# Performance work log

Hardware: AMD Instinct MI355X
Metric: run time of the kernel (lower is better)

The kernel has to match this reference:

```python
import jax, jax.numpy as jnp
import numpy as np

N = 50000
E = 800000
IN, EMB1, EMB2, L1 = 256, 128, 64, 64
EPS = 1e-8


def leaky_relu(x, slope=0.2):
    return jnp.where(x > 0, x, slope * x)


def graph_conv(x, row, col, w_rel, w_root, b):
    # torch_geometric GraphConv with sum aggregation:
    # out = (A @ x) @ w_rel^T + b + x @ w_root^T, where (A @ x)[r] = sum_{e: row[e]=r} x[col[e]]
    agg = jax.ops.segment_sum(x[col], row, num_segments=N)
    return agg @ w_rel.T + x @ w_root.T + b


def setup_inputs() -> dict:
    key = jax.random.key(0)
    ks = jax.random.split(key, 24)
    def g(k, shape, scale=0.05):
        return jax.random.normal(k, shape, dtype=jnp.float32) * scale
    return {
        "x": jax.random.normal(ks[0], (N, IN), dtype=jnp.float32),
        "row": jax.random.randint(ks[1], (E,), 0, N),
        "col": jax.random.randint(ks[2], (E,), 0, N),
        "w_rel1": g(ks[3], (EMB1, IN)), "w_root1": g(ks[4], (EMB1, IN)), "b1": g(ks[5], (EMB1,)),
        "w_rel_mu": g(ks[6], (EMB2, EMB1)), "w_root_mu": g(ks[7], (EMB2, EMB1)), "b_mu": g(ks[8], (EMB2,)),
        "w_std": g(ks[9], (EMB2, EMB1)), "b_std": g(ks[10], (EMB2,)),
        "w_rel_g1": g(ks[11], (L1, EMB2)), "w_root_g1": g(ks[12], (L1, EMB2)), "b_g1": g(ks[13], (L1,)),
        "w_rel_g2": g(ks[14], (1, L1)), "w_root_g2": g(ks[15], (1, L1)), "b_g2": g(ks[16], (1,)),
        "w_cls1": g(ks[17], (L1, EMB2)), "b_cls1": g(ks[18], (L1,)),
        "w_cls2": g(ks[19], (2, L1)), "b_cls2": g(ks[20], (2,)),
        "log_std": jnp.zeros((1,), dtype=jnp.float32),
    }


def reference(x, row, col,
              w_rel1, w_root1, b1,
              w_rel_mu, w_root_mu, b_mu,
              w_std, b_std,
              w_rel_g1, w_root_g1, b_g1,
              w_rel_g2, w_root_g2, b_g2,
              w_cls1, b_cls1, w_cls2, b_cls2, log_std):
    # ----- encode -----
    h = leaky_relu(graph_conv(x, row, col, w_rel1, w_root1, b1))  # [N, EMB1]
    z_mu = jnp.tanh(graph_conv(h, row, col, w_rel_mu, w_root_mu, b_mu))  # [N, EMB2]
    z_log_std = jnp.tanh(h @ w_std.T + b_std)                    # [N, EMB2]
    z_std = jnp.exp(z_log_std)
    z = z_mu  # eval mode
    # ----- decode: per-edge cosine similarity -----
    a, b = z[row], z[col]                                        # [E, EMB2]
    num = jnp.sum(a * b, axis=-1)
    na = jnp.maximum(jnp.linalg.norm(a, axis=-1), EPS)
    nb = jnp.maximum(jnp.linalg.norm(b, axis=-1), EPS)
    w_mu = num / (na * nb)                                       # [E]
    w_std_out = jnp.exp(log_std)                                 # [1]
    # ----- attention pooling -----
    g1 = leaky_relu(graph_conv(z, row, col, w_rel_g1, w_root_g1, b_g1))  # [N, L1]
    gate = graph_conv(g1, row, col, w_rel_g2, w_root_g2, b_g2)   # [N, 1]
    gate = jax.nn.softmax(gate, axis=0)
    pooled = gate.T @ z                                          # [1, EMB2]
    # ----- classifier -----
    y = leaky_relu(pooled @ w_cls1.T + b_cls1)
    y = y @ w_cls2.T + b_cls2
    y = jax.nn.softmax(y, axis=1)                                # [1, 2]
    return (y, w_mu, w_std_out, z, z_mu, z_std)
```

## Files before the change

kernel.cpp:

```cpp
#include <hip/hip_runtime.h>

#define NN 50000
#define EE 800000

__global__ void hist_k(const int* __restrict__ row, int* __restrict__ deg, int E) {
    int e = blockIdx.x * blockDim.x + threadIdx.x;
    if (e < E) atomicAdd(&deg[row[e]], 1);
}

__global__ __launch_bounds__(1024) void scan_k(const int* __restrict__ deg, int* __restrict__ ptr,
                                               int* __restrict__ cursor, int N) {
    __shared__ int sm[1024];
    int t = threadIdx.x;
    int chunk = (N + 1023) / 1024;
    int lo = t * chunk, hi = lo + chunk; if (hi > N) hi = N;
    int s = 0;
    for (int i = lo; i < hi; i++) s += deg[i];
    sm[t] = s;
    __syncthreads();
    for (int off = 1; off < 1024; off <<= 1) {
        int v = (t >= off) ? sm[t - off] : 0;
        __syncthreads();
        sm[t] += v;
        __syncthreads();
    }
    int run = (t == 0) ? 0 : sm[t - 1];
    for (int i = lo; i < hi; i++) { ptr[i] = run; cursor[i] = run; run += deg[i]; }
    if (t == 1023) ptr[N] = sm[1023];
}

__global__ void place_k(const int* __restrict__ row, const int* __restrict__ col,
                        int* __restrict__ cursor, int* __restrict__ ccol, int E) {
    int e = blockIdx.x * blockDim.x + threadIdx.x;
    if (e >= E) return;
    int p = atomicAdd(&cursor[row[e]], 1);
    ccol[p] = col[e];
}

__global__ void transpose_all(const float* __restrict__ w_rel1, const float* __restrict__ w_root1,
                              const float* __restrict__ w_rel_mu, const float* __restrict__ w_root_mu,
                              const float* __restrict__ w_std,
                              const float* __restrict__ w_rel_g1, const float* __restrict__ w_root_g1,
                              float* __restrict__ wt1, float* __restrict__ wt3,
                              float* __restrict__ wtg) {
    int idx = blockIdx.x * 256 + threadIdx.x;
    if (idx < 65536) {
        int j = idx & 255, k = idx >> 8;
        wt1[idx] = (j < 128) ? w_rel1[j * 256 + k] : w_root1[(j - 128) * 256 + k];
    } else if (idx < 90112) {
        int o = idx - 65536; int j = o % 192, k = o / 192;
        wt3[o] = (j < 64) ? w_rel_mu[j * 128 + k]
               : (j < 128) ? w_root_mu[(j - 64) * 128 + k]
                           : w_std[(j - 128) * 128 + k];
    } else if (idx < 98304) {
        int o = idx - 90112; int j = o & 127, k = o >> 7;
        wtg[o] = (j < 64) ? w_rel_g1[j * 64 + k] : w_root_g1[(j - 64) * 64 + k];
    }
}

__global__ __launch_bounds__(64) void mm256_k(const float* __restrict__ x,
        const float* __restrict__ wt,
        float* __restrict__ xr, float* __restrict__ xroot) {
    int t = threadIdx.x;
    int n0 = blockIdx.x * 8;
    const float* xp = x + (size_t)n0 * 256;
    float a0[8] = {}, a1[8] = {}, a2[8] = {}, a3[8] = {};
#pragma unroll 4
    for (int k = 0; k < 256; k++) {
        const float* wk = wt + k * 256;
        float w0 = wk[t], w1 = wk[t + 64], w2 = wk[t + 128], w3 = wk[t + 192];
#pragma unroll
        for (int n = 0; n < 8; n++) {
            float xv = xp[n * 256 + k];
            a0[n] = fmaf(xv, w0, a0[n]);
            a1[n] = fmaf(xv, w1, a1[n]);
            a2[n] = fmaf(xv, w2, a2[n]);
            a3[n] = fmaf(xv, w3, a3[n]);
        }
    }
#pragma unroll
    for (int n = 0; n < 8; n++) {
        size_t o = (size_t)(n0 + n) * 128;
        xr[o + t]        = a0[n];
        xr[o + t + 64]   = a1[n];
        xroot[o + t]      = a2[n];
        xroot[o + t + 64] = a3[n];
    }
}

__global__ __launch_bounds__(128) void agg_k128(const float* __restrict__ src,
        const int* __restrict__ ptr, const int* __restrict__ ccol, float* __restrict__ dst) {
    int r = blockIdx.x, j = threadIdx.x;
    int beg = ptr[r], end = ptr[r + 1];
    float a0 = 0.f, a1 = 0.f, a2 = 0.f, a3 = 0.f;
    int e = beg;
    for (; e + 4 <= end; e += 4) {
        int c0 = ccol[e], c1 = ccol[e + 1], c2 = ccol[e + 2], c3 = ccol[e + 3];
        a0 += src[(size_t)c0 * 128 + j];
        a1 += src[(size_t)c1 * 128 + j];
        a2 += src[(size_t)c2 * 128 + j];
        a3 += src[(size_t)c3 * 128 + j];
    }
    for (; e < end; e++) a0 += src[(size_t)ccol[e] * 128 + j];
    dst[(size_t)r * 128 + j] = (a0 + a1) + (a2 + a3);
}

__global__ __launch_bounds__(256) void h_k(const float4* __restrict__ agg1,
        const float4* __restrict__ xroot, const float* __restrict__ b1,
        float4* __restrict__ h, int total4) {
    int i = blockIdx.x * 256 + threadIdx.x;
    if (i >= total4) return;
    float4 a = agg1[i], x = xroot[i];
    int k = (i & 31) * 4;
    float4 r;
    r.x = a.x + x.x + b1[k + 0]; r.x = r.x > 0.f ? r.x : 0.2f * r.x;
    r.y = a.y + x.y + b1[k + 1]; r.y = r.y > 0.f ? r.y : 0.2f * r.y;
    r.z = a.z + x.z + b1[k + 2]; r.z = r.z > 0.f ? r.z : 0.2f * r.z;
    r.w = a.w + x.w + b1[k + 3]; r.w = r.w > 0.f ? r.w : 0.2f * r.w;
    h[i] = r;
}

__global__ __launch_bounds__(64) void mm128x3_k(const float* __restrict__ h,
        const float* __restrict__ wt,
        float* __restrict__ hr, float* __restrict__ hmu, float* __restrict__ hstd) {
    int t = threadIdx.x;
    int n0 = blockIdx.x * 8;
    const float* hp = h + (size_t)n0 * 128;
    float a0[8] = {}, a1[8] = {}, a2[8] = {};
#pragma unroll 4
    for (int k = 0; k < 128; k++) {
        const float* wk = wt + k * 192;
        float w0 = wk[t], w1 = wk[t + 64], w2 = wk[t + 128];
#pragma unroll
        for (int n = 0; n < 8; n++) {
            float hv = hp[n * 128 + k];
            a0[n] = fmaf(hv, w0, a0[n]);
            a1[n] = fmaf(hv, w1, a1[n]);
            a2[n] = fmaf(hv, w2, a2[n]);
        }
    }
#pragma unroll
    for (int n = 0; n < 8; n++) {
        size_t o = (size_t)(n0 + n) * 64 + t;
        hr[o] = a0[n]; hmu[o] = a1[n]; hstd[o] = a2[n];
    }
}

__global__ __launch_bounds__(64) void aggz_k(const float* __restrict__ hr,
        const float* __restrict__ hmu, const float* __restrict__ hstd,
        const float* __restrict__ b_mu, const float* __restrict__ b_std,
        const int* __restrict__ ptr, const int* __restrict__ ccol,
        float* __restrict__ z, float* __restrict__ out_z, float* __restrict__ out_zmu,
        float* __restrict__ out_zstd, float* __restrict__ nrm) {
    int r = blockIdx.x, j = threadIdx.x;
    int beg = ptr[r], end = ptr[r + 1];
    float a0 = 0.f, a1 = 0.f, a2 = 0.f, a3 = 0.f;
    int e = beg;
    for (; e + 4 <= end; e += 4) {
        int c0 = ccol[e], c1 = ccol[e + 1], c2 = ccol[e + 2], c3 = ccol[e + 3];
        a0 += hr[(size_t)c0 * 64 + j];
        a1 += hr[(size_t)c1 * 64 + j];
        a2 += hr[(size_t)c2 * 64 + j];
        a3 += hr[(size_t)c3 * 64 + j];
    }
    for (; e < end; e++) a0 += hr[(size_t)ccol[e] * 64 + j];
    float acc = (a0 + a1) + (a2 + a3);
    float zmu = tanhf(acc + hmu[(size_t)r * 64 + j] + b_mu[j]);
    float zls = tanhf(hstd[(size_t)r * 64 + j] + b_std[j]);
    float zstd = expf(zls);
    size_t o = (size_t)r * 64 + j;
    z[o] = zmu; out_z[o] = zmu; out_zmu[o] = zmu; out_zstd[o] = zstd;
    float s = zmu * zmu;
    s += __shfl_xor(s, 1); s += __shfl_xor(s, 2); s += __shfl_xor(s, 4);
    s += __shfl_xor(s, 8); s += __shfl_xor(s, 16); s += __shfl_xor(s, 32);
    if (j == 0) nrm[r] = fmaxf(sqrtf(s), 1e-8f);
}

__global__ __launch_bounds__(256) void edge_k(const float* __restrict__ z, const float* __restrict__ nrm,
        const int* __restrict__ row, const int* __restrict__ col, float* __restrict__ out, int E) {
    int t = threadIdx.x;
    int sub = t >> 4, off = t & 15;
    int e = blockIdx.x * 16 + sub;
    if (e >= E) return;
    int r = row[e], c = col[e];
    const float4* a = reinterpret_cast<const float4*>(z + (size_t)r * 64);
    const float4* b = reinterpret_cast<const float4*>(z + (size_t)c * 64);
    float4 av = a[off], bv = b[off];
    float s = av.x * bv.x + av.y * bv.y + av.z * bv.z + av.w * bv.w;
    s += __shfl_xor(s, 1); s += __shfl_xor(s, 2); s += __shfl_xor(s, 4); s += __shfl_xor(s, 8);
    if (off == 0) out[e] = s / (nrm[r] * nrm[c]);
}

__global__ __launch_bounds__(64) void mm64x2_k(const float* __restrict__ z,
        const float* __restrict__ wt,
        float* __restrict__ zr, float* __restrict__ zroot) {
    int t = threadIdx.x;
    int n0 = blockIdx.x * 8;
    const float* zp = z + (size_t)n0 * 64;
    float a0[8] = {}, a1[8] = {};
#pragma unroll 4
    for (int k = 0; k < 64; k++) {
        const float* wk = wt + k * 128;
        float w0 = wk[t], w1 = wk[t + 64];
#pragma unroll
        for (int n = 0; n < 8; n++) {
            float zv = zp[n * 64 + k];
            a0[n] = fmaf(zv, w0, a0[n]);
            a1[n] = fmaf(zv, w1, a1[n]);
        }
    }
#pragma unroll
    for (int n = 0; n < 8; n++) {
        size_t o = (size_t)(n0 + n) * 64 + t;
        zr[o] = a0[n]; zroot[o] = a1[n];
    }
}

__global__ __launch_bounds__(64) void g1gate_k(const float* __restrict__ zr, const float* __restrict__ zroot,
        const float* __restrict__ b_g1, const float* __restrict__ w_rel_g2,
        const float* __restrict__ w_root_g2,
        const int* __restrict__ ptr, const int* __restrict__ ccol,
        float* __restrict__ g1r, float* __restrict__ groot) {
    int r = blockIdx.x, j = threadIdx.x;
    int beg = ptr[r], end = ptr[r + 1];
    float a0 = 0.f, a1 = 0.f, a2 = 0.f, a3 = 0.f;
    int e = beg;
    for (; e + 4 <= end; e += 4) {
        int c0 = ccol[e], c1 = ccol[e + 1], c2 = ccol[e + 2], c3 = ccol[e + 3];
        a0 += zr[(size_t)c0 * 64 + j];
        a1 += zr[(size_t)c1 * 64 + j];
        a2 += zr[(size_t)c2 * 64 + j];
        a3 += zr[(size_t)c3 * 64 + j];
    }
    for (; e < end; e++) a0 += zr[(size_t)ccol[e] * 64 + j];
    float g = (a0 + a1) + (a2 + a3) + zroot[(size_t)r * 64 + j] + b_g1[j];
    g = g > 0.f ? g : 0.2f * g;
    float sr = g * w_rel_g2[j];
    float so = g * w_root_g2[j];
    sr += __shfl_xor(sr, 1); sr += __shfl_xor(sr, 2); sr += __shfl_xor(sr, 4);
    sr += __shfl_xor(sr, 8); sr += __shfl_xor(sr, 16); sr += __shfl_xor(sr, 32);
    so += __shfl_xor(so, 1); so += __shfl_xor(so, 2); so += __shfl_xor(so, 4);
    so += __shfl_xor(so, 8); so += __shfl_xor(so, 16); so += __shfl_xor(so, 32);
    if (j == 0) { g1r[r] = sr; groot[r] = so; }
}

__global__ __launch_bounds__(256) void gateagg_k(const float* __restrict__ g1r,
        const float* __restrict__ groot, const float* __restrict__ b_g2,
        const int* __restrict__ ptr, const int* __restrict__ ccol,
        float* __restrict__ gate, float* __restrict__ pmax, int N) {
    __shared__ float sm[256];
    float b = b_g2[0];
    float m = -3.4e38f;
    for (int r = blockIdx.x * blockDim.x + threadIdx.x; r < N; r += gridDim.x * blockDim.x) {
        int beg = ptr[r], end = ptr[r + 1];
        float s0 = 0.f, s1 = 0.f, s2 = 0.f, s3 = 0.f;
        int e = beg;
        for (; e + 4 <= end; e += 4) {
            s0 += g1r[ccol[e]]; s1 += g1r[ccol[e + 1]];
            s2 += g1r[ccol[e + 2]]; s3 += g1r[ccol[e + 3]];
        }
        for (; e < end; e++) s0 += g1r[ccol[e]];
        float g = (s0 + s1) + (s2 + s3) + groot[r] + b;
        gate[r] = g;
        m = fmaxf(m, g);
    }
    sm[threadIdx.x] = m;
    __syncthreads();
    for (int s2 = 128; s2 > 0; s2 >>= 1) {
        if (threadIdx.x < s2) sm[threadIdx.x] = fmaxf(sm[threadIdx.x], sm[threadIdx.x + s2]);
        __syncthreads();
    }
    if (threadIdx.x == 0) pmax[blockIdx.x] = sm[0];
}

__global__ void reduce_max_final(const float* __restrict__ pmax, float* __restrict__ smax) {
    float m = pmax[threadIdx.x];
    for (int o = 32; o > 0; o >>= 1) m = fmaxf(m, __shfl_down(m, o));
    if (threadIdx.x == 0) smax[0] = m;
}

__global__ __launch_bounds__(256) void pooled_kernel(const float* __restrict__ gate,
        const float* __restrict__ smax, const float* __restrict__ z,
        float* __restrict__ pooled_num, float* __restrict__ wsum, int N) {
    int tid = threadIdx.x;
    int sub = tid >> 6, j = tid & 63;
    float mx = smax[0];
    float acc = 0.f, wsl = 0.f;
    for (int n = blockIdx.x * 4 + sub; n < N; n += gridDim.x * 4) {
        float w = expf(gate[n] - mx);
        acc = fmaf(w, z[(size_t)n * 64 + j], acc);
        if (j == 0) wsl += w;
    }
    __shared__ float lp[4][64];
    __shared__ float lw[4];
    lp[sub][j] = acc;
    if (j == 0) lw[sub] = wsl;
    __syncthreads();
    if (sub == 0) {
        float t = lp[0][j] + lp[1][j] + lp[2][j] + lp[3][j];
        atomicAdd(&pooled_num[j], t);
        if (j == 0) atomicAdd(wsum, lw[0] + lw[1] + lw[2] + lw[3]);
    }
}

__global__ void final_kernel(const float* __restrict__ pooled_num, const float* __restrict__ wsum,
                             const float* __restrict__ w_cls1, const float* __restrict__ b_cls1,
                             const float* __restrict__ w_cls2, const float* __restrict__ b_cls2,
                             const float* __restrict__ log_std,
                             float* __restrict__ out_y, float* __restrict__ out_wstd) {
    __shared__ float sp[64];
    __shared__ float st[64];
    int j = threadIdx.x;
    sp[j] = pooled_num[j] / wsum[0];
    __syncthreads();
    float acc = 0.f;
    const float* w = w_cls1 + j * 64;
#pragma unroll
    for (int k = 0; k < 64; k++) acc = fmaf(sp[k], w[k], acc);
    acc += b_cls1[j];
    st[j] = acc > 0.f ? acc : 0.2f * acc;
    __syncthreads();
    if (j == 0) {
        float l0 = b_cls2[0], l1 = b_cls2[1];
        for (int k = 0; k < 64; k++) {
            l0 = fmaf(st[k], w_cls2[k], l0);
            l1 = fmaf(st[k], w_cls2[64 + k], l1);
        }
        float m = fmaxf(l0, l1);
        float e0 = expf(l0 - m), e1 = expf(l1 - m);
        float s = e0 + e1;
        out_y[0] = e0 / s;
        out_y[1] = e1 / s;
        out_wstd[0] = expf(log_std[0]);
    }
}

extern "C" void kernel_launch(void* const* d_in, const int* in_sizes, int n_in,
                              void* d_out, int out_size, void* d_ws, size_t ws_size,
                              hipStream_t stream) {
    const int N = NN, E = EE;
    const float* x        = (const float*)d_in[0];
    const int*   row      = (const int*)d_in[1];
    const int*   col      = (const int*)d_in[2];
    const float* w_rel1   = (const float*)d_in[3];
    const float* w_root1  = (const float*)d_in[4];
    const float* b1       = (const float*)d_in[5];
    const float* w_rel_mu = (const float*)d_in[6];
    const float* w_root_mu= (const float*)d_in[7];
    const float* b_mu     = (const float*)d_in[8];
    const float* w_std    = (const float*)d_in[9];
    const float* b_std    = (const float*)d_in[10];
    const float* w_rel_g1 = (const float*)d_in[11];
    const float* w_root_g1= (const float*)d_in[12];
    const float* b_g1     = (const float*)d_in[13];
    const float* w_rel_g2 = (const float*)d_in[14];
    const float* w_root_g2= (const float*)d_in[15];
    const float* b_g2     = (const float*)d_in[16];
    const float* w_cls1   = (const float*)d_in[17];
    const float* b_cls1   = (const float*)d_in[18];
    const float* w_cls2   = (const float*)d_in[19];
    const float* b_cls2   = (const float*)d_in[20];
    const float* log_std  = (const float*)d_in[21];

    float* out = (float*)d_out;
    const long long OFF_WMU  = 2;
    const long long OFF_WSTD = 2 + (long long)E;
    const long long OFF_Z    = 3 + (long long)E;
    const long long OFF_ZMU  = OFF_Z + (long long)N * 64;
    const long long OFF_ZSTD = OFF_ZMU + (long long)N * 64;

    float* wsp = (float*)d_ws;
    float* R0   = wsp;
    float* R1   = R0 + (size_t)N * 128;
    float* R2   = R1 + (size_t)N * 128;
    float* R3   = R2 + (size_t)N * 128;
    float* R4   = R3 + (size_t)N * 64;
    float* R5   = R4 + (size_t)4 * N;
    float* wt1  = R5 + 256;
    float* wt3  = wt1 + 65536;
    float* wtg  = wt3 + 24576;
    int*   deg    = (int*)(wtg + 8192);
    int*   ptr    = deg + N;
    int*   cursor = ptr + N + 64;
    int*   ccol   = cursor + N;

    float* xr    = R0;
    float* h     = R0;
    float* xroot = R1;
    float* hr    = R1;
    float* hmu   = R1 + (size_t)N * 64;
    float* agg1  = R2;
    float* hstd  = R2;
    float* zr    = R2;
    float* zroot = R2 + (size_t)N * 64;
    float* zbuf  = R3;
    float* nrm   = R4;
    float* g1r   = R4 + N;
    float* groot = R4 + 2 * (size_t)N;
    float* gate  = R4 + 3 * (size_t)N;
    float* pmax  = R5;
    float* smax  = R5 + 64;
    float* pooled= R5 + 128;
    float* wsum  = R5 + 192;

    hipMemsetAsync(deg, 0, (size_t)N * 4, stream);
    hist_k<<<(E + 255) / 256, 256, 0, stream>>>(row, deg, E);
    scan_k<<<1, 1024, 0, stream>>>(deg, ptr, cursor, N);
    place_k<<<(E + 255) / 256, 256, 0, stream>>>(row, col, cursor, ccol, E);

    transpose_all<<<384, 256, 0, stream>>>(w_rel1, w_root1, w_rel_mu, w_root_mu, w_std,
                                           w_rel_g1, w_root_g1, wt1, wt3, wtg);

    mm256_k<<<N / 8, 64, 0, stream>>>(x, wt1, xr, xroot);
    agg_k128<<<N, 128, 0, stream>>>(xr, ptr, ccol, agg1);
    h_k<<<(N * 128 / 4 + 255) / 256, 256, 0, stream>>>(
        (const float4*)agg1, (const float4*)xroot, b1, (float4*)h, N * 128 / 4);

    mm128x3_k<<<N / 8, 64, 0, stream>>>(h, wt3, hr, hmu, hstd);

    aggz_k<<<N, 64, 0, stream>>>(hr, hmu, hstd, b_mu, b_std, ptr, ccol,
                                 zbuf, out + OFF_Z, out + OFF_ZMU, out + OFF_ZSTD, nrm);

    edge_k<<<(E + 15) / 16, 256, 0, stream>>>(zbuf, nrm, row, col, out + OFF_WMU, E);

    mm64x2_k<<<N / 8, 64, 0, stream>>>(zbuf, wtg, zr, zroot);
    g1gate_k<<<N, 64, 0, stream>>>(zr, zroot, b_g1, w_rel_g2, w_root_g2, ptr, ccol, g1r, groot);
    gateagg_k<<<64, 256, 0, stream>>>(g1r, groot, b_g2, ptr, ccol, gate, pmax, N);
    reduce_max_final<<<1, 64, 0, stream>>>(pmax, smax);
    hipMemsetAsync(pooled, 0, 65 * 4, stream);
    pooled_kernel<<<128, 256, 0, stream>>>(gate, smax, zbuf, pooled, wsum, N);

    final_kernel<<<1, 64, 0, stream>>>(pooled, wsum, w_cls1, b_cls1, w_cls2, b_cls2, log_std,
                                       out, out + OFF_WSTD);
}
```

Measured before the change: 776.7 us.

## Vectorize dense matmuls with k-interleaved float4 weights and fuse aggregation with activation

Weight transposes now interleave four k values per output column so the matmul kernels can load weights and inputs as float4. Each block now handles 16 nodes instead of 8, doubling weight reuse per load. The first-layer aggregation and the bias plus leaky-relu kernel are fused into one float2 kernel, removing a full N×128 intermediate round trip. Buffer aliasing is rearranged to fit the fused kernel. Risks are higher register pressure from 64 accumulators and fewer blocks in flight.

```diff
diff --git a/kernel.cpp b/kernel.cpp
--- a/kernel.cpp
+++ b/kernel.cpp
@@ -45,102 +45,111 @@
                               float* __restrict__ wtg) {
     int idx = blockIdx.x * 256 + threadIdx.x;
     if (idx < 65536) {
-        int j = idx & 255, k = idx >> 8;
-        wt1[idx] = (j < 128) ? w_rel1[j * 256 + k] : w_root1[(j - 128) * 256 + k];
+        int k = idx >> 8, j = idx & 255;
+        int o = (k >> 2) * 1024 + j * 4 + (k & 3);
+        wt1[o] = (j < 128) ? w_rel1[j * 256 + k] : w_root1[(j - 128) * 256 + k];
     } else if (idx < 90112) {
-        int o = idx - 65536; int j = o % 192, k = o / 192;
+        int q = idx - 65536; int k = q / 192, j = q % 192;
+        int o = (k >> 2) * 768 + j * 4 + (k & 3);
         wt3[o] = (j < 64) ? w_rel_mu[j * 128 + k]
                : (j < 128) ? w_root_mu[(j - 64) * 128 + k]
                            : w_std[(j - 128) * 128 + k];
     } else if (idx < 98304) {
-        int o = idx - 90112; int j = o & 127, k = o >> 7;
+        int q = idx - 90112; int k = q >> 7, j = q & 127;
+        int o = (k >> 2) * 512 + j * 4 + (k & 3);
         wtg[o] = (j < 64) ? w_rel_g1[j * 64 + k] : w_root_g1[(j - 64) * 64 + k];
     }
 }
 
 __global__ __launch_bounds__(64) void mm256_k(const float* __restrict__ x,
-        const float* __restrict__ wt,
+        const float4* __restrict__ wt4,
         float* __restrict__ xr, float* __restrict__ xroot) {
     int t = threadIdx.x;
-    int n0 = blockIdx.x * 8;
-    const float* xp = x + (size_t)n0 * 256;
-    float a0[8] = {}, a1[8] = {}, a2[8] = {}, a3[8] = {};
-#pragma unroll 4
-    for (int k = 0; k < 256; k++) {
-        const float* wk = wt + k * 256;
-        float w0 = wk[t], w1 = wk[t + 64], w2 = wk[t + 128], w3 = wk[t + 192];
-#pragma unroll
-        for (int n = 0; n < 8; n++) {
-            float xv = xp[n * 256 + k];
-            a0[n] = fmaf(xv, w0, a0[n]);
-            a1[n] = fmaf(xv, w1, a1[n]);
-            a2[n] = fmaf(xv, w2, a2[n]);
-            a3[n] = fmaf(xv, w3, a3[n]);
+    int n0 = blockIdx.x * 16;
+    const float4* xp = reinterpret_cast<const float4*>(x + (size_t)n0 * 256);
+    float a0[16] = {}, a1[16] = {}, a2[16] = {}, a3[16] = {};
+    for (int k4 = 0; k4 < 64; k4++) {
+        float4 w0 = wt4[k4 * 256 + t];
+        float4 w1 = wt4[k4 * 256 + t + 64];
+        float4 w2 = wt4[k4 * 256 + t + 128];
+        float4 w3 = wt4[k4 * 256 + t + 192];
+#pragma unroll
+        for (int n = 0; n < 16; n++) {
+            float4 xv = xp[n * 64 + k4];
+            a0[n] = fmaf(xv.x, w0.x, a0[n]); a0[n] = fmaf(xv.y, w0.y, a0[n]);
+            a0[n] = fmaf(xv.z, w0.z, a0[n]); a0[n] = fmaf(xv.w, w0.w, a0[n]);
+            a1[n] = fmaf(xv.x, w1.x, a1[n]); a1[n] = fmaf(xv.y, w1.y, a1[n]);
+            a1[n] = fmaf(xv.z, w1.z, a1[n]); a1[n] = fmaf(xv.w, w1.w, a1[n]);
+            a2[n] = fmaf(xv.x, w2.x, a2[n]); a2[n] = fmaf(xv.y, w2.y, a2[n]);
+            a2[n] = fmaf(xv.z, w2.z, a2[n]); a2[n] = fmaf(xv.w, w2.w, a2[n]);
+            a3[n] = fmaf(xv.x, w3.x, a3[n]); a3[n] = fmaf(xv.y, w3.y, a3[n]);
+            a3[n] = fmaf(xv.z, w3.z, a3[n]); a3[n] = fmaf(xv.w, w3.w, a3[n]);
         }
     }
 #pragma unroll
-    for (int n = 0; n < 8; n++) {
+    for (int n = 0; n < 16; n++) {
         size_t o = (size_t)(n0 + n) * 128;
-        xr[o + t]        = a0[n];
-        xr[o + t + 64]   = a1[n];
+        xr[o + t]         = a0[n];
+        xr[o + t + 64]    = a1[n];
         xroot[o + t]      = a2[n];
         xroot[o + t + 64] = a3[n];
     }
 }
 
-__global__ __launch_bounds__(128) void agg_k128(const float* __restrict__ src,
-        const int* __restrict__ ptr, const int* __restrict__ ccol, float* __restrict__ dst) {
+__global__ __launch_bounds__(64) void aggh_k(const float2* __restrict__ xr2,
+        const float2* __restrict__ xroot2, const float* __restrict__ b1,
+        const int* __restrict__ ptr, const int* __restrict__ ccol,
+        float2* __restrict__ h2) {
     int r = blockIdx.x, j = threadIdx.x;
     int beg = ptr[r], end = ptr[r + 1];
-    float a0 = 0.f, a1 = 0.f, a2 = 0.f, a3 = 0.f;
+    float sx0 = 0.f, sy0 = 0.f, sx1 = 0.f, sy1 = 0.f;
+    float sx2 = 0.f, sy2 = 0.f, sx3 = 0.f, sy3 = 0.f;
     int e = beg;
     for (; e + 4 <= end; e += 4) {
         int c0 = ccol[e], c1 = ccol[e + 1], c2 = ccol[e + 2], c3 = ccol[e + 3];
-        a0 += src[(size_t)c0 * 128 + j];
-        a1 += src[(size_t)c1 * 128 + j];
-        a2 += src[(size_t)c2 * 128 + j];
-        a3 += src[(size_t)c3 * 128 + j];
-    }
-    for (; e < end; e++) a0 += src[(size_t)ccol[e] * 128 + j];
-    dst[(size_t)r * 128 + j] = (a0 + a1) + (a2 + a3);
-}
-
-__global__ __launch_bounds__(256) void h_k(const float4* __restrict__ agg1,
-        const float4* __restrict__ xroot, const float* __restrict__ b1,
-        float4* __restrict__ h, int total4) {
-    int i = blockIdx.x * 256 + threadIdx.x;
-    if (i >= total4) return;
-    float4 a = agg1[i], x = xroot[i];
-    int k = (i & 31) * 4;
-    float4 r;
-    r.x = a.x + x.x + b1[k + 0]; r.x = r.x > 0.f ? r.x : 0.2f * r.x;
-    r.y = a.y + x.y + b1[k + 1]; r.y = r.y > 0.f ? r.y : 0.2f * r.y;
-    r.z = a.z + x.z + b1[k + 2]; r.z = r.z > 0.f ? r.z : 0.2f * r.z;
-    r.w = a.w + x.w + b1[k + 3]; r.w = r.w > 0.f ? r.w : 0.2f * r.w;
-    h[i] = r;
+        float2 v0 = xr2[(size_t)c0 * 64 + j];
+        float2 v1 = xr2[(size_t)c1 * 64 + j];
+        float2 v2 = xr2[(size_t)c2 * 64 + j];
+        float2 v3 = xr2[(size_t)c3 * 64 + j];
+        sx0 += v0.x; sy0 += v0.y; sx1 += v1.x; sy1 += v1.y;
+        sx2 += v2.x; sy2 += v2.y; sx3 += v3.x; sy3 += v3.y;
+    }
+    for (; e < end; e++) {
+        float2 v = xr2[(size_t)ccol[e] * 64 + j];
+        sx0 += v.x; sy0 += v.y;
+    }
+    float2 xo = xroot2[(size_t)r * 64 + j];
+    float hx = (sx0 + sx1) + (sx2 + sx3) + xo.x + b1[2 * j];
+    float hy = (sy0 + sy1) + (sy2 + sy3) + xo.y + b1[2 * j + 1];
+    hx = hx > 0.f ? hx : 0.2f * hx;
+    hy = hy > 0.f ? hy : 0.2f * hy;
+    h2[(size_t)r * 64 + j] = make_float2(hx, hy);
 }
 
 __global__ __launch_bounds__(64) void mm128x3_k(const float* __restrict__ h,
-        const float* __restrict__ wt,
+        const float4* __restrict__ wt4,
         float* __restrict__ hr, float* __restrict__ hmu, float* __restrict__ hstd) {
     int t = threadIdx.x;
-    int n0 = blockIdx.x * 8;
-    const float* hp = h + (size_t)n0 * 128;
-    float a0[8] = {}, a1[8] = {}, a2[8] = {};
-#pragma unroll 4
-    for (int k = 0; k < 128; k++) {
-        const float* wk = wt + k * 192;
-        float w0 = wk[t], w1 = wk[t + 64], w2 = wk[t + 128];
-#pragma unroll
-        for (int n = 0; n < 8; n++) {
-            float hv = hp[n * 128 + k];
-            a0[n] = fmaf(hv, w0, a0[n]);
-            a1[n] = fmaf(hv, w1, a1[n]);
-            a2[n] = fmaf(hv, w2, a2[n]);
+    int n0 = blockIdx.x * 16;
+    const float4* hp = reinterpret_cast<const float4*>(h + (size_t)n0 * 128);
+    float a0[16] = {}, a1[16] = {}, a2[16] = {};
+    for (int k4 = 0; k4 < 32; k4++) {
+        float4 w0 = wt4[k4 * 192 + t];
+        float4 w1 = wt4[k4 * 192 + t + 64];
+        float4 w2 = wt4[k4 * 192 + t + 128];
+#pragma unroll
+        for (int n = 0; n < 16; n++) {
+            float4 hv = hp[n * 32 + k4];
+            a0[n] = fmaf(hv.x, w0.x, a0[n]); a0[n] = fmaf(hv.y, w0.y, a0[n]);
+            a0[n] = fmaf(hv.z, w0.z, a0[n]); a0[n] = fmaf(hv.w, w0.w, a0[n]);
+            a1[n] = fmaf(hv.x, w1.x, a1[n]); a1[n] = fmaf(hv.y, w1.y, a1[n]);
+            a1[n] = fmaf(hv.z, w1.z, a1[n]); a1[n] = fmaf(hv.w, w1.w, a1[n]);
+            a2[n] = fmaf(hv.x, w2.x, a2[n]); a2[n] = fmaf(hv.y, w2.y, a2[n]);
+            a2[n] = fmaf(hv.z, w2.z, a2[n]); a2[n] = fmaf(hv.w, w2.w, a2[n]);
         }
     }
 #pragma unroll
-    for (int n = 0; n < 8; n++) {
+    for (int n = 0; n < 16; n++) {
         size_t o = (size_t)(n0 + n) * 64 + t;
         hr[o] = a0[n]; hmu[o] = a1[n]; hstd[o] = a2[n];
     }
@@ -192,25 +201,26 @@
 }
 
 __global__ __launch_bounds__(64) void mm64x2_k(const float* __restrict__ z,
-        const float* __restrict__ wt,
+        const float4* __restrict__ wt4,
         float* __restrict__ zr, float* __restrict__ zroot) {
     int t = threadIdx.x;
-    int n0 = blockIdx.x * 8;
-    const float* zp = z + (size_t)n0 * 64;
-    float a0[8] = {}, a1[8] = {};
-#pragma unroll 4
-    for (int k = 0; k < 64; k++) {
-        const float* wk = wt + k * 128;
-        float w0 = wk[t], w1 = wk[t + 64];
-#pragma unroll
-        for (int n = 0; n < 8; n++) {
-            float zv = zp[n * 64 + k];
-            a0[n] = fmaf(zv, w0, a0[n]);
-            a1[n] = fmaf(zv, w1, a1[n]);
+    int n0 = blockIdx.x * 16;
+    const float4* zp = reinterpret_cast<const float4*>(z + (size_t)n0 * 64);
+    float a0[16] = {}, a1[16] = {};
+    for (int k4 = 0; k4 < 16; k4++) {
+        float4 w0 = wt4[k4 * 128 + t];
+        float4 w1 = wt4[k4 * 128 + t + 64];
+#pragma unroll
+        for (int n = 0; n < 16; n++) {
+            float4 zv = zp[n * 16 + k4];
+            a0[n] = fmaf(zv.x, w0.x, a0[n]); a0[n] = fmaf(zv.y, w0.y, a0[n]);
+            a0[n] = fmaf(zv.z, w0.z, a0[n]); a0[n] = fmaf(zv.w, w0.w, a0[n]);
+            a1[n] = fmaf(zv.x, w1.x, a1[n]); a1[n] = fmaf(zv.y, w1.y, a1[n]);
+            a1[n] = fmaf(zv.z, w1.z, a1[n]); a1[n] = fmaf(zv.w, w1.w, a1[n]);
         }
     }
 #pragma unroll
-    for (int n = 0; n < 8; n++) {
+    for (int n = 0; n < 16; n++) {
         size_t o = (size_t)(n0 + n) * 64 + t;
         zr[o] = a0[n]; zroot[o] = a1[n];
     }
@@ -385,12 +395,11 @@
     int*   ccol   = cursor + N;
 
     float* xr    = R0;
-    float* h     = R0;
+    float* hstd  = R0;
     float* xroot = R1;
     float* hr    = R1;
     float* hmu   = R1 + (size_t)N * 64;
-    float* agg1  = R2;
-    float* hstd  = R2;
+    float* h     = R2;
     float* zr    = R2;
     float* zroot = R2 + (size_t)N * 64;
     float* zbuf  = R3;
@@ -411,19 +420,18 @@
     transpose_all<<<384, 256, 0, stream>>>(w_rel1, w_root1, w_rel_mu, w_root_mu, w_std,
                                            w_rel_g1, w_root_g1, wt1, wt3, wtg);
 
-    mm256_k<<<N / 8, 64, 0, stream>>>(x, wt1, xr, xroot);
-    agg_k128<<<N, 128, 0, stream>>>(xr, ptr, ccol, agg1);
-    h_k<<<(N * 128 / 4 + 255) / 256, 256, 0, stream>>>(
-        (const float4*)agg1, (const float4*)xroot, b1, (float4*)h, N * 128 / 4);
-
-    mm128x3_k<<<N / 8, 64, 0, stream>>>(h, wt3, hr, hmu, hstd);
+    mm256_k<<<N / 16, 64, 0, stream>>>(x, (const float4*)wt1, xr, xroot);
+    aggh_k<<<N, 64, 0, stream>>>((const float2*)xr, (const float2*)xroot, b1, ptr, ccol,
+                                 (float2*)h);
+
+    mm128x3_k<<<N / 16, 64, 0, stream>>>(h, (const float4*)wt3, hr, hmu, hstd);
 
     aggz_k<<<N, 64, 0, stream>>>(hr, hmu, hstd, b_mu, b_std, ptr, ccol,
                                  zbuf, out + OFF_Z, out + OFF_ZMU, out + OFF_ZSTD, nrm);
 
     edge_k<<<(E + 15) / 16, 256, 0, stream>>>(zbuf, nrm, row, col, out + OFF_WMU, E);
 
-    mm64x2_k<<<N / 8, 64, 0, stream>>>(zbuf, wtg, zr, zroot);
+    mm64x2_k<<<N / 16, 64, 0, stream>>>(zbuf, (const float4*)wtg, zr, zroot);
     g1gate_k<<<N, 64, 0, stream>>>(zr, zroot, b_g1, w_rel_g2, w_root_g2, ptr, ccol, g1r, groot);
     gateagg_k<<<64, 256, 0, stream>>>(g1r, groot, b_g2, ptr, ccol, gate, pmax, N);
     reduce_max_final<<<1, 64, 0, stream>>>(pmax, smax);
```

New measurement: 791.5 us. Within noise of the previous version (+1.9%).
